# Performance work log

Hardware: AMD Instinct MI355X
Metric: run time of the kernel (lower is better)

Reference implementation:

```python
import jax, jax.numpy as jnp
import numpy as np

DIM = 1024
MEM_DIM = 1024
BANK = 8192
B, S = 4, 4096
LN_EPS = 1e-5


def setup_inputs() -> dict:
    key = jax.random.key(0)
    ks = jax.random.split(key, 8)
    std_q = 1.0 / np.sqrt(DIM)
    std_m = 1.0 / np.sqrt(MEM_DIM)
    std_f = 1.0 / np.sqrt(DIM + MEM_DIM)
    return {
        "x": jax.random.normal(ks[0], (B, S, DIM), jnp.float32),
        "knowledge_bank": 0.02 * jax.random.normal(ks[1], (BANK, MEM_DIM), jnp.float32),
        "wq": std_q * jax.random.normal(ks[2], (MEM_DIM, DIM), jnp.float32),
        "bq": jnp.zeros((MEM_DIM,), jnp.float32),
        "wk": std_m * jax.random.normal(ks[3], (MEM_DIM, MEM_DIM), jnp.float32),
        "bk": jnp.zeros((MEM_DIM,), jnp.float32),
        "wv": std_m * jax.random.normal(ks[4], (DIM, MEM_DIM), jnp.float32),
        "bv": jnp.zeros((DIM,), jnp.float32),
        "wf": std_f * jax.random.normal(ks[5], (DIM, DIM + MEM_DIM), jnp.float32),
        "bf": jnp.zeros((DIM,), jnp.float32),
        "gamma": jnp.ones((DIM,), jnp.float32),
        "beta": jnp.zeros((DIM,), jnp.float32),
    }


def reference(x, knowledge_bank, wq, bq, wk, bk, wv, bv, wf, bf, gamma, beta):
    # queries: [B,S,MEM_DIM]; keys/values over the fixed bank: [BANK, *]
    queries = jnp.einsum("bsd,md->bsm", x, wq) + bq
    keys = jnp.einsum("nd,md->nm", knowledge_bank, wk) + bk
    values = jnp.einsum("nd,md->nm", knowledge_bank, wv) + bv
    scores = jnp.einsum("bsm,nm->bsn", queries, keys) / jnp.sqrt(
        jnp.asarray(MEM_DIM, x.dtype)
    )
    attn = jax.nn.softmax(scores, axis=-1)  # [B,S,BANK]
    retrieved = jnp.einsum("bsn,nd->bsd", attn, values)  # [B,S,DIM]
    combined = jnp.concatenate([x, retrieved], axis=-1)  # [B,S,2*DIM]
    out = jnp.einsum("bsc,dc->bsd", combined, wf) + bf
    h = out + x
    # LayerNorm over last dim, eps = 1e-5 (torch default)
    mu = jnp.mean(h, axis=-1, keepdims=True)
    var = jnp.mean(jnp.square(h - mu), axis=-1, keepdims=True)
    return (h - mu) * jax.lax.rsqrt(var + LN_EPS) * gamma + beta
```

## Files before the change

### kernel.cpp

```cpp
#include <hip/hip_runtime.h>


typedef __bf16 bf16;
typedef __bf16 bf16x4 __attribute__((ext_vector_type(4)));
typedef __bf16 bf16x8 __attribute__((ext_vector_type(8)));
typedef float f32x4 __attribute__((ext_vector_type(4)));

static __device__ __forceinline__ f32x4 mfma16(bf16x8 a, bf16x8 b, f32x4 c) {
  return __builtin_amdgcn_mfma_f32_16x16x32_bf16(a, b, c, 0, 0, 0);
}

#define GLDS16(gp, lp) __builtin_amdgcn_global_load_lds( \
    (const __attribute__((address_space(1))) void*)(gp), \
    (__attribute__((address_space(3))) void*)(lp), 16, 0, 0)

template<int EPI, int CONCAT, int XMAP>
__global__ __launch_bounds__(256, 3) void gemm_bb(
    const bf16* __restrict__ A, const bf16* __restrict__ A2,
    const bf16* __restrict__ W, const float* __restrict__ bias,
    const float* __restrict__ resid, float* __restrict__ L,
    void* __restrict__ Cout, int N, int K, int ldw)
{
  __shared__ bf16 As[128 * 64];
  __shared__ bf16 Bs[128 * 64];
  const int tid = threadIdx.x, lane = tid & 63, wid = tid >> 6;
  const int wm = (wid >> 1) * 64, wn = (wid & 1) * 64;
  const int quad = lane >> 4, l16 = lane & 15;
  long bm, bn;
  if (XMAP == 1) {
    const int flat = (int)(blockIdx.y * gridDim.x + blockIdx.x);
    const int xcd = flat & 7;
    const int idx = flat >> 3;
    const int nbxl = (int)gridDim.x >> 3;
    const int byp = idx / nbxl;
    const int bxl = idx - byp * nbxl;
    bm = (long)byp * 128;
    bn = (long)(xcd * nbxl + bxl) * 128;
  } else {
    const int nwg = (int)(gridDim.x * gridDim.y);
    int flat = (int)(blockIdx.y * gridDim.x + blockIdx.x);
    flat = (flat & 7) * (nwg >> 3) + (flat >> 3);
    bm = (long)(flat / (int)gridDim.x) * 128;
    bn = (long)(flat % (int)gridDim.x) * 128;
  }

  int prow[4], pcg[4];
#pragma unroll
  for (int i = 0; i < 4; ++i) {
    int p = ((wid * 4 + i) << 6) + lane;
    prow[i] = p >> 3;
    pcg[i] = (p & 7) ^ (prow[i] & 7);
  }

  f32x4 acc[4][4] = {};

  for (int k0 = 0; k0 < K; k0 += 64) {
    const bf16* Asrc = (CONCAT && k0 >= 1024) ? A2 : A;
    const int kA = (CONCAT && k0 >= 1024) ? k0 - 1024 : k0;
    const int lda = CONCAT ? 1024 : K;
    __syncthreads();
#pragma unroll
    for (int i = 0; i < 4; ++i) {
      const bf16* ga = Asrc + (size_t)(bm + prow[i]) * lda + kA + pcg[i] * 8;
      GLDS16(ga, (char*)As + ((wid * 4 + i) << 10));
    }
#pragma unroll
    for (int i = 0; i < 4; ++i) {
      const bf16* gb = W + (size_t)(bn + prow[i]) * ldw + k0 + pcg[i] * 8;
      GLDS16(gb, (char*)Bs + ((wid * 4 + i) << 10));
    }
    __syncthreads();
#pragma unroll
    for (int kk = 0; kk < 2; ++kk) {
      bf16x8 af[4], bfv[4];
#pragma unroll
      for (int mt = 0; mt < 4; ++mt) {
        const int r = wm + mt * 16 + l16;
        af[mt] = *(const bf16x8*)((const char*)As + (r << 7)
                                  + ((((kk << 2) + quad) ^ (r & 7)) << 4));
      }
#pragma unroll
      for (int nt = 0; nt < 4; ++nt) {
        const int r = wn + nt * 16 + l16;
        bfv[nt] = *(const bf16x8*)((const char*)Bs + (r << 7)
                                   + ((((kk << 2) + quad) ^ (r & 7)) << 4));
      }
#pragma unroll
      for (int mt = 0; mt < 4; ++mt)
#pragma unroll
        for (int nt = 0; nt < 4; ++nt)
          acc[mt][nt] = mfma16(af[mt], bfv[nt], acc[mt][nt]);
    }
  }

#pragma unroll
  for (int mt = 0; mt < 4; ++mt) {
    const long row0 = bm + wm + mt * 16 + quad * 4;
    if (EPI == 2) {
      float rsum[4] = {0.f, 0.f, 0.f, 0.f};
#pragma unroll
      for (int nt = 0; nt < 4; ++nt) {
        const long col = bn + wn + nt * 16 + l16;
#pragma unroll
        for (int r = 0; r < 4; ++r) {
          float p = __expf(acc[mt][nt][r] * 0.03125f);
          rsum[r] += p;
          ((bf16*)Cout)[(size_t)(row0 + r) * N + col] = (bf16)p;
        }
      }
#pragma unroll
      for (int s = 1; s < 16; s <<= 1)
#pragma unroll
        for (int r = 0; r < 4; ++r) rsum[r] += __shfl_xor(rsum[r], s, 64);
      if (l16 == 0) {
#pragma unroll
        for (int r = 0; r < 4; ++r) atomicAdd(&L[row0 + r], rsum[r]);
      }
    } else {
#pragma unroll
      for (int nt = 0; nt < 4; ++nt) {
        const long col = bn + wn + nt * 16 + l16;
        const float bc = (EPI == 1) ? 0.f : bias[col];
#pragma unroll
        for (int r = 0; r < 4; ++r) {
          float v = acc[mt][nt][r] + ((EPI == 1) ? bias[row0 + r] : bc);
          if (EPI == 3) {
            v += resid[(size_t)(row0 + r) * 1024 + col];
            ((float*)Cout)[(size_t)(row0 + r) * N + col] = v;
          } else {
            ((bf16*)Cout)[(size_t)(row0 + r) * N + col] = (bf16)v;
          }
        }
      }
    }
  }
}

__global__ __launch_bounds__(512, 2) void pv_gemm(
    const bf16* __restrict__ P, const bf16* __restrict__ Vt,
    const float* __restrict__ L, bf16* __restrict__ Rb)
{
  __shared__ bf16 As[4][128 * 64];
  __shared__ bf16 Bs[4][128 * 64];
  const int tid = threadIdx.x, lane = tid & 63, wid = tid >> 6;
  const int wm = (wid & 3) * 32, wn = (wid >> 2) * 64;
  const int quad = lane >> 4, l16 = lane & 15;
  long bm, bn;
  {
    const int nwg = (int)(gridDim.x * gridDim.y);
    int flat = (int)(blockIdx.y * gridDim.x + blockIdx.x);
    flat = (flat & 7) * (nwg >> 3) + (flat >> 3);
    bm = (long)(flat / (int)gridDim.x) * 128;
    bn = (long)(flat % (int)gridDim.x) * 128;
  }

  int prow[2], pcg[2];
#pragma unroll
  for (int i = 0; i < 2; ++i) {
    int p = ((wid * 2 + i) << 6) + lane;
    prow[i] = p >> 3;
    pcg[i] = (p & 7) ^ (prow[i] & 7);
  }

  f32x4 acc[2][4] = {};

  auto stage = [&](int buf, int k0) {
#pragma unroll
    for (int i = 0; i < 2; ++i)
      GLDS16(P + (size_t)(bm + prow[i]) * 8192 + k0 + pcg[i] * 8,
             (char*)As[buf] + ((wid * 2 + i) << 10));
#pragma unroll
    for (int i = 0; i < 2; ++i)
      GLDS16(Vt + (size_t)(bn + prow[i]) * 8192 + k0 + pcg[i] * 8,
             (char*)Bs[buf] + ((wid * 2 + i) << 10));
  };

  auto compute = [&](int buf) {
    __builtin_amdgcn_s_setprio(1);
#pragma unroll
    for (int kk = 0; kk < 2; ++kk) {
      bf16x8 af[2], bfv[4];
#pragma unroll
      for (int mt = 0; mt < 2; ++mt) {
        const int r = wm + mt * 16 + l16;
        af[mt] = *(const bf16x8*)((const char*)As[buf] + (r << 7)
                                  + ((((kk << 2) + quad) ^ (r & 7)) << 4));
      }
#pragma unroll
      for (int nt = 0; nt < 4; ++nt) {
        const int r = wn + nt * 16 + l16;
        bfv[nt] = *(const bf16x8*)((const char*)Bs[buf] + (r << 7)
                                   + ((((kk << 2) + quad) ^ (r & 7)) << 4));
      }
#pragma unroll
      for (int mt = 0; mt < 2; ++mt)
#pragma unroll
        for (int nt = 0; nt < 4; ++nt)
          acc[mt][nt] = mfma16(af[mt], bfv[nt], acc[mt][nt]);
    }
    __builtin_amdgcn_s_setprio(0);
  };

  stage(0, 0);
  stage(1, 64);
  stage(2, 128);
  for (int t = 0; t < 126; ++t) {
    asm volatile("s_waitcnt vmcnt(8)" ::: "memory");
    __builtin_amdgcn_s_barrier();
    compute(t & 3);
    if (t < 125) stage((t + 3) & 3, (t + 3) * 64);
  }
  asm volatile("s_waitcnt vmcnt(4)" ::: "memory");
  __builtin_amdgcn_s_barrier();
  compute(126 & 3);
  asm volatile("s_waitcnt vmcnt(0)" ::: "memory");
  __builtin_amdgcn_s_barrier();
  compute(127 & 3);

#pragma unroll
  for (int mt = 0; mt < 2; ++mt) {
    const long row0 = bm + wm + mt * 16 + quad * 4;
    float linv[4];
#pragma unroll
    for (int r = 0; r < 4; ++r) linv[r] = 1.f / L[row0 + r];
#pragma unroll
    for (int nt = 0; nt < 4; ++nt) {
      const long col = bn + wn + nt * 16 + l16;
#pragma unroll
      for (int r = 0; r < 4; ++r)
        Rb[(size_t)(row0 + r) * 1024 + col] = (bf16)(acc[mt][nt][r] * linv[r]);
    }
  }
}

template<int BIAS_ROW, int OUT_F32_RES, int CONCAT>
__global__ __launch_bounds__(256, 3) void gemm_nt(
    const float* __restrict__ A, const bf16* __restrict__ A2,
    const float* __restrict__ W, const float* __restrict__ bias,
    const float* __restrict__ resid, void* __restrict__ Cout,
    int M, int N, int K)
{
  __shared__ bf16 As[128][72];
  __shared__ bf16 Bs[128][72];
  const int tid  = threadIdx.x;
  const int lane = tid & 63;
  const int wid  = tid >> 6;
  const int wm   = (wid >> 1) * 64, wn = (wid & 1) * 64;
  const int quad = lane >> 4, l16 = lane & 15;
  const long bm = (long)blockIdx.y * 128, bn = (long)blockIdx.x * 128;
  const int r0 = tid >> 2, cq = (tid & 3) * 16;
  const int lda = CONCAT ? 1024 : K;

  f32x4 acc[4][4] = {};

  for (int k0 = 0; k0 < K; k0 += 64) {
    const bool useb = CONCAT && (k0 >= 1024);
    const int kA = useb ? (k0 - 1024) : k0;
    f32x4 va[2][4], vb[2][4];
    bf16x8 ra[2][2];
    if (useb) {
#pragma unroll
      for (int g = 0; g < 2; ++g) {
        const bf16* p = A2 + (size_t)(bm + r0 + 64 * g) * 1024 + kA + cq;
        ra[g][0] = *(const bf16x8*)p;
        ra[g][1] = *(const bf16x8*)(p + 8);
      }
    } else {
#pragma unroll
      for (int g = 0; g < 2; ++g) {
        const f32x4* p = (const f32x4*)(A + (size_t)(bm + r0 + 64 * g) * lda + kA + cq);
#pragma unroll
        for (int j = 0; j < 4; ++j) va[g][j] = p[j];
      }
    }
#pragma unroll
    for (int g = 0; g < 2; ++g) {
      const f32x4* p = (const f32x4*)(W + (size_t)(bn + r0 + 64 * g) * K + k0 + cq);
#pragma unroll
      for (int j = 0; j < 4; ++j) vb[g][j] = p[j];
    }
    __syncthreads();
#pragma unroll
    for (int g = 0; g < 2; ++g) {
      bf16* dA = &As[r0 + 64 * g][cq];
      if (useb) {
        *(bf16x8*)dA = ra[g][0]; *(bf16x8*)(dA + 8) = ra[g][1];
      } else {
        bf16x8 t0, t1;
#pragma unroll
        for (int j = 0; j < 4; ++j) {
          t0[j] = (bf16)va[g][0][j]; t0[4 + j] = (bf16)va[g][1][j];
          t1[j] = (bf16)va[g][2][j]; t1[4 + j] = (bf16)va[g][3][j];
        }
        *(bf16x8*)dA = t0; *(bf16x8*)(dA + 8) = t1;
      }
      bf16* dB = &Bs[r0 + 64 * g][cq];
      bf16x8 u0, u1;
#pragma unroll
      for (int j = 0; j < 4; ++j) {
        u0[j] = (bf16)vb[g][0][j]; u0[4 + j] = (bf16)vb[g][1][j];
        u1[j] = (bf16)vb[g][2][j]; u1[4 + j] = (bf16)vb[g][3][j];
      }
      *(bf16x8*)dB = u0; *(bf16x8*)(dB + 8) = u1;
    }
    __syncthreads();
#pragma unroll
    for (int kk = 0; kk < 2; ++kk) {
      bf16x8 af[4], bfv[4];
#pragma unroll
      for (int mt = 0; mt < 4; ++mt)
        af[mt] = *(const bf16x8*)&As[wm + mt * 16 + l16][kk * 32 + quad * 8];
#pragma unroll
      for (int nt = 0; nt < 4; ++nt)
        bfv[nt] = *(const bf16x8*)&Bs[wn + nt * 16 + l16][kk * 32 + quad * 8];
#pragma unroll
      for (int mt = 0; mt < 4; ++mt)
#pragma unroll
        for (int nt = 0; nt < 4; ++nt)
          acc[mt][nt] = mfma16(af[mt], bfv[nt], acc[mt][nt]);
    }
  }
#pragma unroll
  for (int mt = 0; mt < 4; ++mt) {
    const long row0 = bm + wm + mt * 16 + quad * 4;
#pragma unroll
    for (int nt = 0; nt < 4; ++nt) {
      const long col = bn + wn + nt * 16 + l16;
      const float bc = BIAS_ROW ? 0.f : bias[col];
#pragma unroll
      for (int r = 0; r < 4; ++r) {
        float v = acc[mt][nt][r] + (BIAS_ROW ? bias[row0 + r] : bc);
        if (OUT_F32_RES) {
          v += resid[(size_t)(row0 + r) * 1024 + col];
          ((float*)Cout)[(size_t)(row0 + r) * N + col] = v;
        } else {
          ((bf16*)Cout)[(size_t)(row0 + r) * N + col] = (bf16)v;
        }
      }
    }
  }
}

__global__ __launch_bounds__(256) void cvt6(
    const float* __restrict__ x, const float* __restrict__ bank,
    const float* __restrict__ wq, const float* __restrict__ wk,
    const float* __restrict__ wv, const float* __restrict__ wf,
    bf16* __restrict__ xb, bf16* __restrict__ bankb,
    bf16* __restrict__ wqb, bf16* __restrict__ wkb,
    bf16* __restrict__ wvb, bf16* __restrict__ wfb)
{
  long i4 = (long)blockIdx.x * 256 + threadIdx.x;
  const float* src; bf16* dst; long off;
  if      (i4 < 4194304) { src = x;    dst = xb;    off = i4; }
  else if (i4 < 6291456) { src = bank; dst = bankb; off = i4 - 4194304; }
  else if (i4 < 6553600) { src = wq;   dst = wqb;   off = i4 - 6291456; }
  else if (i4 < 6815744) { src = wk;   dst = wkb;   off = i4 - 6553600; }
  else if (i4 < 7077888) { src = wv;   dst = wvb;   off = i4 - 6815744; }
  else if (i4 < 7602176) { src = wf;   dst = wfb;   off = i4 - 7077888; }
  else return;
  f32x4 v = ((const f32x4*)src)[off];
  bf16x4 o;
#pragma unroll
  for (int j = 0; j < 4; ++j) o[j] = (bf16)v[j];
  ((bf16x4*)dst)[off] = o;
}

__global__ __launch_bounds__(256) void zerof(float* __restrict__ p) {
  p[(size_t)blockIdx.x * 256 + threadIdx.x] = 0.f;
}

__global__ __launch_bounds__(256) void ln_kernel(
    float* __restrict__ h, const float* __restrict__ g, const float* __restrict__ b)
{
  const int tid = threadIdx.x;
  const size_t row = blockIdx.x;
  f32x4 v = *(f32x4*)&h[row * 1024 + tid * 4];
  float s1 = v[0] + v[1] + v[2] + v[3];
  float s2 = v[0]*v[0] + v[1]*v[1] + v[2]*v[2] + v[3]*v[3];
#pragma unroll
  for (int d = 1; d < 64; d <<= 1) { s1 += __shfl_xor(s1, d, 64); s2 += __shfl_xor(s2, d, 64); }
  __shared__ float a1[4], a2[4];
  const int wid = tid >> 6;
  if ((tid & 63) == 0) { a1[wid] = s1; a2[wid] = s2; }
  __syncthreads();
  s1 = a1[0] + a1[1] + a1[2] + a1[3];
  s2 = a2[0] + a2[1] + a2[2] + a2[3];
  const float mu = s1 * (1.f / 1024.f);
  const float rs = rsqrtf(s2 * (1.f / 1024.f) - mu * mu + 1e-5f);
  f32x4 gv = *(const f32x4*)&g[tid * 4];
  f32x4 bv = *(const f32x4*)&b[tid * 4];
#pragma unroll
  for (int j = 0; j < 4; ++j) v[j] = (v[j] - mu) * rs * gv[j] + bv[j];
  *(f32x4*)&h[row * 1024 + tid * 4] = v;
}

extern "C" void kernel_launch(void* const* d_in, const int* in_sizes, int n_in,
                              void* d_out, int out_size, void* d_ws, size_t ws_size,
                              hipStream_t stream)
{
  const float* x     = (const float*)d_in[0];
  const float* kbank = (const float*)d_in[1];
  const float* wq    = (const float*)d_in[2];
  const float* bq    = (const float*)d_in[3];
  const float* wk    = (const float*)d_in[4];
  const float* bk    = (const float*)d_in[5];
  const float* wv    = (const float*)d_in[6];
  const float* bv    = (const float*)d_in[7];
  const float* wf    = (const float*)d_in[8];
  const float* bf_   = (const float*)d_in[9];
  const float* gamma = (const float*)d_in[10];
  const float* beta  = (const float*)d_in[11];

  char* ws = (char*)d_ws;
  const size_t MB = 1024 * 1024;
  bf16*  Qb    = (bf16*)ws;
  bf16*  Rb    = Qb;
  bf16*  Kb    = (bf16*)(ws + 32 * MB);
  bf16*  Vt    = (bf16*)(ws + 48 * MB);
  float* L     = (float*)(ws + 64 * MB);
  bf16*  xb    = (bf16*)(ws + 65 * MB);
  bf16*  bankb = (bf16*)(ws + 97 * MB);
  bf16*  wfb   = (bf16*)(ws + 113 * MB);
  bf16*  wqb   = (bf16*)(ws + 117 * MB);
  bf16*  wkb   = (bf16*)(ws + 119 * MB);
  bf16*  wvb   = (bf16*)(ws + 121 * MB);
  bf16*  P     = (bf16*)d_out;
  float* out   = (float*)d_out;
  const bool big = ws_size >= 123 * MB;

  if (big) {
    cvt6<<<dim3(29696), dim3(256), 0, stream>>>(
        x, kbank, wq, wk, wv, wf, xb, bankb, wqb, wkb, wvb, wfb);
    gemm_bb<0,0,0><<<dim3(8, 128), dim3(256), 0, stream>>>(
        xb, nullptr, wqb, bq, nullptr, nullptr, (void*)Qb, 1024, 1024, 1024);
    gemm_bb<0,0,0><<<dim3(8, 64), dim3(256), 0, stream>>>(
        bankb, nullptr, wkb, bk, nullptr, nullptr, (void*)Kb, 1024, 1024, 1024);
    gemm_bb<1,0,1><<<dim3(64, 8), dim3(256), 0, stream>>>(
        wvb, nullptr, bankb, bv, nullptr, nullptr, (void*)Vt, 8192, 1024, 1024);
  } else {
    gemm_nt<0,0,0><<<dim3(8, 128), dim3(256), 0, stream>>>(
        x, nullptr, wq, bq, nullptr, (void*)Qb, 16384, 1024, 1024);
    gemm_nt<0,0,0><<<dim3(8, 64), dim3(256), 0, stream>>>(
        kbank, nullptr, wk, bk, nullptr, (void*)Kb, 8192, 1024, 1024);
    gemm_nt<1,0,0><<<dim3(64, 8), dim3(256), 0, stream>>>(
        wv, nullptr, kbank, bv, nullptr, (void*)Vt, 1024, 8192, 1024);
  }

  zerof<<<dim3(64), dim3(256), 0, stream>>>(L);
  for (int c = 0; c < 4; ++c) {
    gemm_bb<2,0,1><<<dim3(64, 32), dim3(256), 0, stream>>>(
        Qb + (size_t)c * 4096 * 1024, nullptr, Kb, nullptr, nullptr,
        L + c * 4096, (void*)P, 8192, 1024, 1024);
    pv_gemm<<<dim3(8, 32), dim3(512), 0, stream>>>(
        P, Vt, L + c * 4096, Rb + (size_t)c * 4096 * 1024);
  }

  if (big) {
    gemm_bb<3,1,0><<<dim3(8, 128), dim3(256), 0, stream>>>(
        xb, Rb, wfb, bf_, x, nullptr, (void*)out, 1024, 2048, 2048);
  } else {
    gemm_nt<0,1,1><<<dim3(8, 128), dim3(256), 0, stream>>>(
        x, Rb, wf, bf_, x, (void*)out, 16384, 1024, 2048);
  }
  ln_kernel<<<dim3(16384), dim3(256), 0, stream>>>(out, gamma, beta);
}
```

Measured before the change: 1.018 ms.

## Double-buffer LDS tiles in bf16 GEMM with async prefetch two stages ahead

Converts the GEMM main loop from single-buffered LDS staging with two syncthreads per step into a double-buffered pipeline. Global-to-LDS loads for tile t+2 are issued while tile t is computed, and partial vmcnt waits replace full barriers. It also raises wave priority around the MFMA block. LDS use doubles and the occupancy hint drops from 3 to 2 blocks per CU. The hand-written vmcnt accounting relies on each thread issuing exactly eight loads per stage.

```diff
diff --git a/kernel.cpp b/kernel.cpp
--- a/kernel.cpp
+++ b/kernel.cpp
@@ -15,14 +15,14 @@
     (__attribute__((address_space(3))) void*)(lp), 16, 0, 0)
 
 template<int EPI, int CONCAT, int XMAP>
-__global__ __launch_bounds__(256, 3) void gemm_bb(
+__global__ __launch_bounds__(256, 2) void gemm_bb(
     const bf16* __restrict__ A, const bf16* __restrict__ A2,
     const bf16* __restrict__ W, const float* __restrict__ bias,
     const float* __restrict__ resid, float* __restrict__ L,
     void* __restrict__ Cout, int N, int K, int ldw)
 {
-  __shared__ bf16 As[128 * 64];
-  __shared__ bf16 Bs[128 * 64];
+  __shared__ bf16 As[2][128 * 64];
+  __shared__ bf16 Bs[2][128 * 64];
   const int tid = threadIdx.x, lane = tid & 63, wid = tid >> 6;
   const int wm = (wid >> 1) * 64, wn = (wid & 1) * 64;
   const int quad = lane >> 4, l16 = lane & 15;
@@ -54,35 +54,37 @@
 
   f32x4 acc[4][4] = {};
 
-  for (int k0 = 0; k0 < K; k0 += 64) {
+  auto stage = [&](int buf, int k0) {
     const bf16* Asrc = (CONCAT && k0 >= 1024) ? A2 : A;
     const int kA = (CONCAT && k0 >= 1024) ? k0 - 1024 : k0;
     const int lda = CONCAT ? 1024 : K;
-    __syncthreads();
 #pragma unroll
     for (int i = 0; i < 4; ++i) {
       const bf16* ga = Asrc + (size_t)(bm + prow[i]) * lda + kA + pcg[i] * 8;
-      GLDS16(ga, (char*)As + ((wid * 4 + i) << 10));
+      GLDS16(ga, (char*)As[buf] + ((wid * 4 + i) << 10));
     }
 #pragma unroll
     for (int i = 0; i < 4; ++i) {
       const bf16* gb = W + (size_t)(bn + prow[i]) * ldw + k0 + pcg[i] * 8;
-      GLDS16(gb, (char*)Bs + ((wid * 4 + i) << 10));
-    }
-    __syncthreads();
+      GLDS16(gb, (char*)Bs[buf] + ((wid * 4 + i) << 10));
+    }
+  };
+
+  auto compute = [&](int buf) {
+    __builtin_amdgcn_s_setprio(1);
 #pragma unroll
     for (int kk = 0; kk < 2; ++kk) {
       bf16x8 af[4], bfv[4];
 #pragma unroll
       for (int mt = 0; mt < 4; ++mt) {
         const int r = wm + mt * 16 + l16;
-        af[mt] = *(const bf16x8*)((const char*)As + (r << 7)
+        af[mt] = *(const bf16x8*)((const char*)As[buf] + (r << 7)
                                   + ((((kk << 2) + quad) ^ (r & 7)) << 4));
       }
 #pragma unroll
       for (int nt = 0; nt < 4; ++nt) {
         const int r = wn + nt * 16 + l16;
-        bfv[nt] = *(const bf16x8*)((const char*)Bs + (r << 7)
+        bfv[nt] = *(const bf16x8*)((const char*)Bs[buf] + (r << 7)
                                    + ((((kk << 2) + quad) ^ (r & 7)) << 4));
       }
 #pragma unroll
@@ -90,6 +92,21 @@
 #pragma unroll
         for (int nt = 0; nt < 4; ++nt)
           acc[mt][nt] = mfma16(af[mt], bfv[nt], acc[mt][nt]);
+    }
+    __builtin_amdgcn_s_setprio(0);
+  };
+
+  const int nk = K >> 6;
+  stage(0, 0);
+  stage(1, 64);
+  for (int t = 0; t < nk; ++t) {
+    if (t + 1 < nk) { asm volatile("s_waitcnt vmcnt(8)" ::: "memory"); }
+    else            { asm volatile("s_waitcnt vmcnt(0)" ::: "memory"); }
+    __builtin_amdgcn_s_barrier();
+    compute(t & 1);
+    if (t + 2 < nk) {
+      __builtin_amdgcn_s_barrier();
+      stage(t & 1, (t + 2) * 64);
     }
   }
 
```

Measured after the change: 1.109 ms. 1.09x slower.

## Add dedicated 256x128-tile score+exp kernel with triple-buffered async LDS loads

Applied to the files above, without the earlier changes.

Replaces the generic gemm_bb score/exp epilogue kernel with a specialized 512-thread kernel using 256x128 output tiles, a three-stage global_load_lds pipeline with manual vmcnt waits, XOR-swizzled LDS, and an XCD-aware block mapping. The larger tile raises arithmetic intensity and cuts redundant Q/K reloads, and the deeper pipeline aims to hide memory latency. It uses much more LDS per block (about 144 KB), which limits occupancy, and it hardcodes the problem dimensions.

```diff
diff --git a/kernel.cpp b/kernel.cpp
--- a/kernel.cpp
+++ b/kernel.cpp
@@ -136,6 +136,116 @@
   }
 }
 
+__global__ __launch_bounds__(512, 2) void sexp256(
+    const bf16* __restrict__ Q, const bf16* __restrict__ Kb,
+    float* __restrict__ L, bf16* __restrict__ P)
+{
+  __shared__ bf16 As[3][256 * 64];
+  __shared__ bf16 Bs[3][128 * 64];
+  const int tid = threadIdx.x, lane = tid & 63, wid = tid >> 6;
+  const int wm = (wid >> 1) * 64, wn = (wid & 1) * 64;
+  const int quad = lane >> 4, l16 = lane & 15;
+  const int flat = (int)(blockIdx.y * 64 + blockIdx.x);
+  const int xcd = flat & 7;
+  const int idx = flat >> 3;
+  const long bm = (long)(idx >> 3) * 256;
+  const long bn = (long)(xcd * 8 + (idx & 7)) * 128;
+
+  int prA[4], pcA[4], prB[2], pcB[2];
+#pragma unroll
+  for (int i = 0; i < 4; ++i) {
+    int p = ((wid * 4 + i) << 6) + lane;
+    prA[i] = p >> 3;
+    pcA[i] = (p & 7) ^ (prA[i] & 7);
+  }
+#pragma unroll
+  for (int i = 0; i < 2; ++i) {
+    int q = ((wid * 2 + i) << 6) + lane;
+    prB[i] = q >> 3;
+    pcB[i] = (q & 7) ^ (prB[i] & 7);
+  }
+
+  f32x4 acc[4][4] = {};
+
+  auto stage = [&](int buf, int k0) {
+#pragma unroll
+    for (int i = 0; i < 4; ++i)
+      GLDS16(Q + (size_t)(bm + prA[i]) * 1024 + k0 + pcA[i] * 8,
+             (char*)As[buf] + ((wid * 4 + i) << 10));
+#pragma unroll
+    for (int i = 0; i < 2; ++i)
+      GLDS16(Kb + (size_t)(bn + prB[i]) * 1024 + k0 + pcB[i] * 8,
+             (char*)Bs[buf] + ((wid * 2 + i) << 10));
+  };
+
+  auto compute = [&](int buf) {
+    __builtin_amdgcn_s_setprio(1);
+#pragma unroll
+    for (int kk = 0; kk < 2; ++kk) {
+      bf16x8 af[4], bfv[4];
+#pragma unroll
+      for (int mt = 0; mt < 4; ++mt) {
+        const int r = wm + mt * 16 + l16;
+        af[mt] = *(const bf16x8*)((const char*)As[buf] + (r << 7)
+                                  + ((((kk << 2) + quad) ^ (r & 7)) << 4));
+      }
+#pragma unroll
+      for (int nt = 0; nt < 4; ++nt) {
+        const int r = wn + nt * 16 + l16;
+        bfv[nt] = *(const bf16x8*)((const char*)Bs[buf] + (r << 7)
+                                   + ((((kk << 2) + quad) ^ (r & 7)) << 4));
+      }
+#pragma unroll
+      for (int mt = 0; mt < 4; ++mt)
+#pragma unroll
+        for (int nt = 0; nt < 4; ++nt)
+          acc[mt][nt] = mfma16(af[mt], bfv[nt], acc[mt][nt]);
+    }
+    __builtin_amdgcn_s_setprio(0);
+  };
+
+  stage(0, 0);
+  stage(1, 64);
+  stage(2, 128);
+  int buf = 0;
+  for (int t = 0; t < 16; ++t) {
+    if (t <= 13)      asm volatile("s_waitcnt vmcnt(12)" ::: "memory");
+    else if (t == 14) asm volatile("s_waitcnt vmcnt(6)" ::: "memory");
+    else              asm volatile("s_waitcnt vmcnt(0)" ::: "memory");
+    __builtin_amdgcn_s_barrier();
+    compute(buf);
+    if (t + 3 < 16) {
+      __builtin_amdgcn_s_barrier();
+      stage(buf, (t + 3) * 64);
+    }
+    buf = (buf == 2) ? 0 : buf + 1;
+  }
+
+#pragma unroll
+  for (int mt = 0; mt < 4; ++mt) {
+    const long row0 = bm + wm + mt * 16 + quad * 4;
+    float rsum[4] = {0.f, 0.f, 0.f, 0.f};
+#pragma unroll
+    for (int nt = 0; nt < 4; ++nt) {
+      const long col = bn + wn + nt * 16 + l16;
+#pragma unroll
+      for (int r = 0; r < 4; ++r) {
+        float p = __expf(acc[mt][nt][r] * 0.03125f);
+        rsum[r] += p;
+        P[(size_t)(row0 + r) * 8192 + col] = (bf16)p;
+      }
+    }
+#pragma unroll
+    for (int s = 1; s < 16; s <<= 1)
+#pragma unroll
+      for (int r = 0; r < 4; ++r) rsum[r] += __shfl_xor(rsum[r], s, 64);
+    if (l16 == 0) {
+#pragma unroll
+      for (int r = 0; r < 4; ++r) atomicAdd(&L[row0 + r], rsum[r]);
+    }
+  }
+}
+
 __global__ __launch_bounds__(512, 2) void pv_gemm(
     const bf16* __restrict__ P, const bf16* __restrict__ Vt,
     const float* __restrict__ L, bf16* __restrict__ Rb)
@@ -448,9 +558,8 @@
 
   zerof<<<dim3(64), dim3(256), 0, stream>>>(L);
   for (int c = 0; c < 4; ++c) {
-    gemm_bb<2,0,1><<<dim3(64, 32), dim3(256), 0, stream>>>(
-        Qb + (size_t)c * 4096 * 1024, nullptr, Kb, nullptr, nullptr,
-        L + c * 4096, (void*)P, 8192, 1024, 1024);
+    sexp256<<<dim3(64, 16), dim3(512), 0, stream>>>(
+        Qb + (size_t)c * 4096 * 1024, Kb, L + c * 4096, P);
     pv_gemm<<<dim3(8, 32), dim3(512), 0, stream>>>(
         P, Vt, L + c * 4096, Rb + (size_t)c * 4096 * 1024);
   }
```

Result: slower. 1.129 ms (+10.9%).
